# Optimization experiments

Measured on AMD Instinct MI355X. Metric: run time of the kernel, lower is better.

The kernel has to match this reference:

```python
import jax, jax.numpy as jnp
import numpy as np
from itertools import permutations

SIZES = (16, 32, 32, 32)  # token_sizes for layout dims (v, t, h, w)
N = SIZES[0] * SIZES[1] * SIZES[2] * SIZES[3]  # num_tokens = 524288
B = 32
EPS = 1e-3


def setup_inputs() -> dict:
    key = jax.random.key(0)
    ks = jax.random.split(key, 12)
    u = lambda k, shape: jax.random.uniform(k, shape, dtype=jnp.float32)
    alphas = [1.0, 2.0, 4.0]
    comps = np.array(
        [[alphas[v], alphas[t], alphas[hw], alphas[hw]]
         for v, t, hw in permutations(range(3), 3)], dtype=np.float32)  # [6, 4]
    return {
        "components": jnp.asarray(comps),
        "u_rate_src": u(ks[0], (1,)),
        "u_rate_tgt": u(ks[1], (1,)),
        "u0_src": u(ks[2], (B, N)),
        "u0_tgt": u(ks[3], (B, N)),
        "u_v_src": u(ks[4], (B, SIZES[0])),
        "u_t_src": u(ks[5], (B, SIZES[1])),
        "u_h_src": u(ks[6], (B, SIZES[2])),
        "u_w_src": u(ks[7], (B, SIZES[3])),
        "u_v_tgt": u(ks[8], (B, SIZES[0])),
        "u_t_tgt": u(ks[9], (B, SIZES[1])),
        "u_h_tgt": u(ks[10], (B, SIZES[2])),
        "u_w_tgt": u(ks[11], (B, SIZES[3])),
        "idx": 2,
    }


def _clamp(x):
    return jnp.clip(x, EPS, 1.0 - EPS)


def _binary_mask(u_rate, u0, u_dims, alphas):
    # event_prior: log-prob per token = log U0 + sum_dim log(U_dim)/alpha_dim (broadcast over pattern)
    P = jnp.log(_clamp(u0))  # [B, N]
    for i, ud in enumerate(u_dims):
        shape = [B, 1, 1, 1, 1]
        shape[1 + i] = SIZES[i]
        rep = jnp.broadcast_to(
            (jnp.log(_clamp(ud)) / alphas[i]).reshape(shape),
            (B,) + SIZES).reshape(B, N)
        P = P + rep
    # rate_prior: one shared uniform, K = floor(U * N), expanded over batch
    K = (_clamp(u_rate) * N).astype(jnp.int32)  # [1]
    K = jnp.broadcast_to(K, (B,))[:, None]  # [B, 1]
    # binary_topk_: rank via double argsort (0 = largest), mask = K > rank
    rank = jnp.argsort(jnp.argsort(-P, axis=-1), axis=-1)
    return K > rank


def reference(components, u_rate_src, u_rate_tgt, u0_src, u0_tgt,
              u_v_src, u_t_src, u_h_src, u_w_src,
              u_v_tgt, u_t_tgt, u_h_tgt, u_w_tgt, idx):
    alphas = components[idx]  # [4], one alpha per layout dim, shared by src/tgt
    src = _binary_mask(u_rate_src, u0_src,
                       (u_v_src, u_t_src, u_h_src, u_w_src), alphas)
    tgt = _binary_mask(u_rate_tgt, u0_tgt,
                       (u_v_tgt, u_t_tgt, u_h_tgt, u_w_tgt), alphas)
    return src, tgt
```

## Files before the change

kernel.cpp:

```cpp
#include <hip/hip_runtime.h>
#include <stdint.h>

#define NTOK 524288
#define ROWS 64
#define CHUNKS 64
#define NTHR 256
#define F4_PER_ROW (NTOK / 4)
#define F4_PER_CHUNK (F4_PER_ROW / CHUNKS)
#define F4_PER_THR (F4_PER_CHUNK / NTHR)
#define GCAP 8192
#define CB1CAP 131072
#define STAGECAP 2048
#define FB_CHUNKS 16

#define OFF_H1   0u
#define OFF_H2   (OFF_H1 + ROWS * 4096u * 4u)
#define OFF_B1   (OFF_H2 + ROWS * 4096u * 4u)
#define OFF_CG   (OFF_B1 + 256u)
#define OFF_B2   (OFF_CG + 256u)
#define OFF_REM  (OFF_B2 + 256u)
#define OFF_IT   (OFF_REM + 256u)
#define OFF_GCNT (OFF_IT + 256u)
#define OFF_BCNT (OFF_GCNT + 256u)
#define OFF_T    (OFF_BCNT + 256u)
#define OFF_ZERO_END (OFF_T + 512u)
#define OFF_TAB  OFF_ZERO_END
#define OFF_BK   (OFF_TAB + ROWS * 112u * 8u)
#define OFF_BI   (OFF_BK + (size_t)ROWS * CB1CAP * 8u)
#define OFF_GKEY (OFF_BI + (size_t)ROWS * CB1CAP * 4u)
#define OFF_GIDX (OFF_GKEY + (size_t)ROWS * GCAP * 8u)

__device__ __forceinline__ double clamp64(double x) {
  return fmin(fmax(x, 1.0e-3), 1.0 - 1.0e-3);
}

__device__ __forceinline__ unsigned compute_K(float ur) {
  float urf = fminf(fmaxf(ur, 1.0e-3f), 1.0f - 1.0e-3f);
  return (unsigned)(int)(urf * (float)NTOK);
}

__global__ void k_tables(const float* __restrict__ comps, const int* __restrict__ idxp,
                         const float* __restrict__ uvs, const float* __restrict__ uts,
                         const float* __restrict__ uhs, const float* __restrict__ uws,
                         const float* __restrict__ uvt, const float* __restrict__ utt,
                         const float* __restrict__ uht, const float* __restrict__ uwt,
                         double* __restrict__ tabs) {
  int idx = idxp[0];
  double alpha[4];
  for (int d = 0; d < 4; ++d) alpha[d] = (double)comps[idx * 4 + d];
  for (int i = threadIdx.x; i < ROWS * 112; i += blockDim.x) {
    int row = i / 112, j = i % 112;
    int m = row >> 5, b = row & 31;
    int d, jj, dsz;
    if (j < 16)      { d = 0; jj = j;      dsz = 16; }
    else if (j < 48) { d = 1; jj = j - 16; dsz = 32; }
    else if (j < 80) { d = 2; jj = j - 48; dsz = 32; }
    else             { d = 3; jj = j - 80; dsz = 32; }
    const float* u;
    if (m == 0) u = (d == 0) ? uvs : (d == 1) ? uts : (d == 2) ? uhs : uws;
    else        u = (d == 0) ? uvt : (d == 1) ? utt : (d == 2) ? uht : uwt;
    double x = clamp64((double)u[b * dsz + jj]);
    double a = alpha[d];
    double f;
    if (a == 1.0)      f = x;
    else if (a == 2.0) f = sqrt(x);
    else if (a == 4.0) f = sqrt(sqrt(x));
    else               f = pow(x, 1.0 / a);
    tabs[row * 112 + j] = f;
  }
}

__global__ void k_hist1(const float* __restrict__ u0s, const float* __restrict__ u0t,
                        const double* __restrict__ tabs, unsigned int* __restrict__ gh1) {
  __shared__ double tb[112];
  __shared__ unsigned int h[2 * 4100];
  int row = blockIdx.x / CHUNKS, chunk = blockIdx.x % CHUNKS;
  for (int i = threadIdx.x; i < 112; i += blockDim.x) tb[i] = tabs[row * 112 + i];
  for (int i = threadIdx.x; i < 2 * 4100; i += blockDim.x) h[i] = 0;
  __syncthreads();
  unsigned rep = (threadIdx.x & 1) * 4100u;
  int m = row >> 5, b = row & 31;
  const float4* u0 = reinterpret_cast<const float4*>((m ? u0t : u0s) + (size_t)b * NTOK);
  int base = chunk * F4_PER_CHUNK;
  for (int it = 0; it < F4_PER_THR; ++it) {
    int f4 = base + it * NTHR + threadIdx.x;
    float4 x = u0[f4];
    int n0 = f4 * 4;
    int w0 = n0 & 31, hh = (n0 >> 5) & 31, tt = (n0 >> 10) & 31, vv = n0 >> 15;
    double g = tb[vv] * tb[16 + tt] * tb[48 + hh];
    double k0 = clamp64((double)x.x) * (g * tb[80 + w0 + 0]);
    double k1 = clamp64((double)x.y) * (g * tb[80 + w0 + 1]);
    double k2 = clamp64((double)x.z) * (g * tb[80 + w0 + 2]);
    double k3 = clamp64((double)x.w) * (g * tb[80 + w0 + 3]);
    atomicAdd(&h[rep + ((unsigned)((unsigned long long)__double_as_longlong(k0) >> 51) & 0xFFFu)], 1u);
    atomicAdd(&h[rep + ((unsigned)((unsigned long long)__double_as_longlong(k1) >> 51) & 0xFFFu)], 1u);
    atomicAdd(&h[rep + ((unsigned)((unsigned long long)__double_as_longlong(k2) >> 51) & 0xFFFu)], 1u);
    atomicAdd(&h[rep + ((unsigned)((unsigned long long)__double_as_longlong(k3) >> 51) & 0xFFFu)], 1u);
  }
  __syncthreads();
  for (int i = threadIdx.x; i < 4096; i += blockDim.x) {
    unsigned c = h[i] + h[4100 + i];
    if (c) atomicAdd(&gh1[row * 4096 + i], c);
  }
}

__global__ __launch_bounds__(256) void k_scan1(const unsigned int* __restrict__ gh1,
                                               const float* __restrict__ urs,
                                               const float* __restrict__ urt,
                                               int* __restrict__ sB1, int* __restrict__ sCG) {
  __shared__ unsigned suf[256];
  __shared__ int best;
  int row = blockIdx.x;
  int t = threadIdx.x;
  const unsigned* h = gh1 + row * 4096;
  unsigned loc[16]; unsigned own = 0;
#pragma unroll
  for (int i = 0; i < 16; ++i) { loc[i] = h[t * 16 + i]; own += loc[i]; }
  suf[t] = own;
  if (t == 0) best = -1;
  __syncthreads();
  for (int off = 1; off < 256; off <<= 1) {
    unsigned add = (t + off < 256) ? suf[t + off] : 0u;
    __syncthreads();
    suf[t] += add;
    __syncthreads();
  }
  int m = row >> 5;
  unsigned K = compute_K(m ? urt[0] : urs[0]);
  unsigned above = suf[t] - own;
  int cand = -1;
  unsigned cum = above;
  for (int i = 15; i >= 0; --i) {
    if (cum + loc[i] >= K) { cand = t * 16 + i; break; }
    cum += loc[i];
  }
  if (cand >= 0) atomicMax(&best, cand);
  __syncthreads();
  int bb = best;
  if (bb >= 0 && (bb >> 4) == t) {
    unsigned cg = above;
    for (int i = 15; i > (bb & 15); --i) cg += loc[i];
    sB1[row] = bb;
    sCG[row] = (int)cg;
  }
}

__global__ void k_hist2g(const float* __restrict__ u0s, const float* __restrict__ u0t,
                         const double* __restrict__ tabs, const int* __restrict__ sB1,
                         unsigned int* __restrict__ gh2,
                         unsigned int* __restrict__ bcnt,
                         unsigned long long* __restrict__ bk, unsigned int* __restrict__ bi) {
  __shared__ double tb[112];
  __shared__ unsigned int h[4096];
  __shared__ unsigned long long sk[STAGECAP];
  __shared__ unsigned int si[STAGECAP];
  __shared__ unsigned int scnt;
  __shared__ unsigned int sbase;
  int row = blockIdx.x / CHUNKS, chunk = blockIdx.x % CHUNKS;
  for (int i = threadIdx.x; i < 112; i += blockDim.x) tb[i] = tabs[row * 112 + i];
  for (int i = threadIdx.x; i < 4096; i += blockDim.x) h[i] = 0;
  if (threadIdx.x == 0) scnt = 0;
  __syncthreads();
  unsigned b1 = (unsigned)sB1[row];
  int m = row >> 5, b = row & 31;
  const float4* u0 = reinterpret_cast<const float4*>((m ? u0t : u0s) + (size_t)b * NTOK);
  int base = chunk * F4_PER_CHUNK;
  for (int it = 0; it < F4_PER_THR; ++it) {
    int f4 = base + it * NTHR + threadIdx.x;
    float4 x = u0[f4];
    int n0 = f4 * 4;
    int w0 = n0 & 31, hh = (n0 >> 5) & 31, tt = (n0 >> 10) & 31, vv = n0 >> 15;
    double g = tb[vv] * tb[16 + tt] * tb[48 + hh];
    double ks[4];
    ks[0] = clamp64((double)x.x) * (g * tb[80 + w0 + 0]);
    ks[1] = clamp64((double)x.y) * (g * tb[80 + w0 + 1]);
    ks[2] = clamp64((double)x.z) * (g * tb[80 + w0 + 2]);
    ks[3] = clamp64((double)x.w) * (g * tb[80 + w0 + 3]);
#pragma unroll
    for (int c = 0; c < 4; ++c) {
      unsigned long long kb = (unsigned long long)__double_as_longlong(ks[c]);
      if (((unsigned)(kb >> 51) & 0xFFFu) == b1) {
        atomicAdd(&h[(unsigned)(kb >> 39) & 0xFFFu], 1u);
        unsigned p = atomicAdd(&scnt, 1u);
        if (p < STAGECAP) { sk[p] = kb; si[p] = (unsigned)(n0 + c); }
        else {
          unsigned gp = atomicAdd(&bcnt[row], 1u);
          if (gp < CB1CAP) {
            bk[(size_t)row * CB1CAP + gp] = kb;
            bi[(size_t)row * CB1CAP + gp] = (unsigned)(n0 + c);
          }
        }
      }
    }
  }
  __syncthreads();
  unsigned nst = scnt; if (nst > STAGECAP) nst = STAGECAP;
  if (threadIdx.x == 0) sbase = atomicAdd(&bcnt[row], nst);
  __syncthreads();
  unsigned bs = sbase;
  for (unsigned i = threadIdx.x; i < nst; i += blockDim.x) {
    unsigned gp = bs + i;
    if (gp < CB1CAP) {
      bk[(size_t)row * CB1CAP + gp] = sk[i];
      bi[(size_t)row * CB1CAP + gp] = si[i];
    }
  }
  for (int i = threadIdx.x; i < 4096; i += blockDim.x) {
    unsigned c = h[i];
    if (c) atomicAdd(&gh2[row * 4096 + i], c);
  }
}

__global__ __launch_bounds__(256) void k_scan2(const unsigned int* __restrict__ gh2,
                                               const float* __restrict__ urs,
                                               const float* __restrict__ urt,
                                               const int* __restrict__ sCG,
                                               int* __restrict__ sB2, int* __restrict__ sREM) {
  __shared__ unsigned suf[256];
  __shared__ int best;
  int row = blockIdx.x;
  int t = threadIdx.x;
  const unsigned* h = gh2 + row * 4096;
  unsigned loc[16]; unsigned own = 0;
#pragma unroll
  for (int i = 0; i < 16; ++i) { loc[i] = h[t * 16 + i]; own += loc[i]; }
  suf[t] = own;
  if (t == 0) best = -1;
  __syncthreads();
  for (int off = 1; off < 256; off <<= 1) {
    unsigned add = (t + off < 256) ? suf[t + off] : 0u;
    __syncthreads();
    suf[t] += add;
    __syncthreads();
  }
  int m = row >> 5;
  unsigned K = compute_K(m ? urt[0] : urs[0]);
  unsigned K2 = K - (unsigned)sCG[row];
  unsigned above = suf[t] - own;
  int cand = -1;
  unsigned cum = above;
  for (int i = 15; i >= 0; --i) {
    if (cum + loc[i] >= K2) { cand = t * 16 + i; break; }
    cum += loc[i];
  }
  if (cand >= 0) atomicMax(&best, cand);
  __syncthreads();
  int bb = best;
  if (bb >= 0 && (bb >> 4) == t) {
    unsigned a2 = above;
    for (int i = 15; i > (bb & 15); --i) a2 += loc[i];
    sB2[row] = bb;
    sREM[row] = (int)(K2 - a2);
  }
}

__global__ void k_gather_fb(const float* __restrict__ u0s, const float* __restrict__ u0t,
                            const double* __restrict__ tabs,
                            const int* __restrict__ sB1, const int* __restrict__ sB2,
                            const unsigned int* __restrict__ bcnt,
                            unsigned int* __restrict__ gcnt,
                            unsigned long long* __restrict__ gkey, unsigned int* __restrict__ gidx) {
  int row = blockIdx.x / FB_CHUNKS, chunk = blockIdx.x % FB_CHUNKS;
  if (bcnt[row] <= CB1CAP) return;
  __shared__ double tb[112];
  for (int i = threadIdx.x; i < 112; i += blockDim.x) tb[i] = tabs[row * 112 + i];
  __syncthreads();
  unsigned pref = ((unsigned)sB1[row] << 12) | (unsigned)sB2[row];
  int m = row >> 5, b = row & 31;
  const float4* u0 = reinterpret_cast<const float4*>((m ? u0t : u0s) + (size_t)b * NTOK);
  int base = chunk * (F4_PER_ROW / FB_CHUNKS);
  for (int it = 0; it < F4_PER_ROW / FB_CHUNKS / NTHR; ++it) {
    int f4 = base + it * NTHR + threadIdx.x;
    float4 x = u0[f4];
    int n0 = f4 * 4;
    int w0 = n0 & 31, hh = (n0 >> 5) & 31, tt = (n0 >> 10) & 31, vv = n0 >> 15;
    double g = tb[vv] * tb[16 + tt] * tb[48 + hh];
    double ks[4];
    ks[0] = clamp64((double)x.x) * (g * tb[80 + w0 + 0]);
    ks[1] = clamp64((double)x.y) * (g * tb[80 + w0 + 1]);
    ks[2] = clamp64((double)x.z) * (g * tb[80 + w0 + 2]);
    ks[3] = clamp64((double)x.w) * (g * tb[80 + w0 + 3]);
#pragma unroll
    for (int c = 0; c < 4; ++c) {
      unsigned long long kb = (unsigned long long)__double_as_longlong(ks[c]);
      if (((unsigned)(kb >> 39) & 0xFFFFFFu) == pref) {
        unsigned pos = atomicAdd(&gcnt[row], 1u);
        if (pos < GCAP) {
          gkey[(size_t)row * GCAP + pos] = kb;
          gidx[(size_t)row * GCAP + pos] = (unsigned)(n0 + c);
        }
      }
    }
  }
}

__global__ __launch_bounds__(1024) void k_select(const unsigned long long* __restrict__ bk,
                                                 const unsigned int* __restrict__ bi,
                                                 const unsigned int* __restrict__ bcnt,
                                                 const unsigned long long* __restrict__ gkey,
                                                 const unsigned int* __restrict__ gidx,
                                                 const unsigned int* __restrict__ gcnt,
                                                 const int* __restrict__ sB2,
                                                 const int* __restrict__ sREM,
                                                 unsigned long long* __restrict__ sT,
                                                 int* __restrict__ sIT) {
  __shared__ unsigned long long k[GCAP];
  __shared__ unsigned int ix[GCAP];
  __shared__ unsigned int lcnt;
  int row = blockIdx.x;
  if (threadIdx.x == 0) lcnt = 0;
  __syncthreads();
  unsigned cnt1 = bcnt[row];
  unsigned n_r;
  if (cnt1 <= CB1CAP) {
    unsigned b2 = (unsigned)sB2[row];
    for (unsigned i = threadIdx.x; i < cnt1; i += blockDim.x) {
      unsigned long long kb = bk[(size_t)row * CB1CAP + i];
      if (((unsigned)(kb >> 39) & 0xFFFu) == b2) {
        unsigned p = atomicAdd(&lcnt, 1u);
        if (p < GCAP) { k[p] = kb; ix[p] = bi[(size_t)row * CB1CAP + i]; }
      }
    }
    __syncthreads();
    n_r = lcnt; if (n_r > GCAP) n_r = GCAP;
  } else {
    n_r = gcnt[row];
    if (n_r > GCAP) n_r = GCAP;
    for (unsigned i = threadIdx.x; i < n_r; i += blockDim.x) {
      k[i] = gkey[(size_t)row * GCAP + i];
      ix[i] = gidx[(size_t)row * GCAP + i];
    }
    __syncthreads();
  }
  unsigned n2 = 2;
  while (n2 < n_r) n2 <<= 1;
  for (unsigned i = threadIdx.x; i < n2; i += blockDim.x) {
    if (i >= n_r) { k[i] = 0ULL; ix[i] = 0xFFFFFFFFu; }
  }
  __syncthreads();
  for (unsigned kk = 2; kk <= n2; kk <<= 1) {
    for (unsigned j = kk >> 1; j > 0; j >>= 1) {
      for (int i = threadIdx.x; i < (int)n2; i += blockDim.x) {
        int pj = i ^ (int)j;
        if (pj > i) {
          unsigned long long k1 = k[i], k2 = k[pj];
          unsigned i1 = ix[i], i2 = ix[pj];
          bool bef = (k1 > k2) || (k1 == k2 && i1 < i2);
          bool dirAsc = ((i & (int)kk) == 0);
          if (bef != dirAsc) { k[i] = k2; k[pj] = k1; ix[i] = i2; ix[pj] = i1; }
        }
      }
      __syncthreads();
    }
  }
  if (threadIdx.x == 0) {
    int rem = sREM[row];
    if (rem < 1) rem = 1;
    if ((unsigned)rem > n_r) rem = (int)n_r;
    sT[row] = k[rem - 1];
    sIT[row] = (int)ix[rem - 1];
  }
}

__global__ void k_final(const float* __restrict__ u0s, const float* __restrict__ u0t,
                        const double* __restrict__ tabs,
                        const unsigned long long* __restrict__ sT, const int* __restrict__ sIT,
                        int* __restrict__ out) {
  __shared__ double tb[112];
  int row = blockIdx.x / CHUNKS, chunk = blockIdx.x % CHUNKS;
  for (int i = threadIdx.x; i < 112; i += blockDim.x) tb[i] = tabs[row * 112 + i];
  __syncthreads();
  unsigned long long T = sT[row];
  int IT = sIT[row];
  int m = row >> 5, b = row & 31;
  const float4* u0 = reinterpret_cast<const float4*>((m ? u0t : u0s) + (size_t)b * NTOK);
  int4* o = reinterpret_cast<int4*>(out + (size_t)row * NTOK);
  int base = chunk * F4_PER_CHUNK;
  for (int it = 0; it < F4_PER_THR; ++it) {
    int f4 = base + it * NTHR + threadIdx.x;
    float4 x = u0[f4];
    int n0 = f4 * 4;
    int w0 = n0 & 31, hh = (n0 >> 5) & 31, tt = (n0 >> 10) & 31, vv = n0 >> 15;
    double g = tb[vv] * tb[16 + tt] * tb[48 + hh];
    unsigned long long kb0 = (unsigned long long)__double_as_longlong(clamp64((double)x.x) * (g * tb[80 + w0 + 0]));
    unsigned long long kb1 = (unsigned long long)__double_as_longlong(clamp64((double)x.y) * (g * tb[80 + w0 + 1]));
    unsigned long long kb2 = (unsigned long long)__double_as_longlong(clamp64((double)x.z) * (g * tb[80 + w0 + 2]));
    unsigned long long kb3 = (unsigned long long)__double_as_longlong(clamp64((double)x.w) * (g * tb[80 + w0 + 3]));
    int4 r;
    r.x = (kb0 > T || (kb0 == T && (n0 + 0) <= IT)) ? 1 : 0;
    r.y = (kb1 > T || (kb1 == T && (n0 + 1) <= IT)) ? 1 : 0;
    r.z = (kb2 > T || (kb2 == T && (n0 + 2) <= IT)) ? 1 : 0;
    r.w = (kb3 > T || (kb3 == T && (n0 + 3) <= IT)) ? 1 : 0;
    o[f4] = r;
  }
}

extern "C" void kernel_launch(void* const* d_in, const int* in_sizes, int n_in,
                              void* d_out, int out_size, void* d_ws, size_t ws_size,
                              hipStream_t stream) {
  const float* comps = (const float*)d_in[0];
  const float* urs   = (const float*)d_in[1];
  const float* urt   = (const float*)d_in[2];
  const float* u0s   = (const float*)d_in[3];
  const float* u0t   = (const float*)d_in[4];
  const float* uvs   = (const float*)d_in[5];
  const float* uts   = (const float*)d_in[6];
  const float* uhs   = (const float*)d_in[7];
  const float* uws   = (const float*)d_in[8];
  const float* uvt   = (const float*)d_in[9];
  const float* utt   = (const float*)d_in[10];
  const float* uht   = (const float*)d_in[11];
  const float* uwt   = (const float*)d_in[12];
  const int*   idxp  = (const int*)d_in[13];
  int* out = (int*)d_out;

  char* ws = (char*)d_ws;
  unsigned int*       gh1  = (unsigned int*)(ws + OFF_H1);
  unsigned int*       gh2  = (unsigned int*)(ws + OFF_H2);
  int*                sB1  = (int*)(ws + OFF_B1);
  int*                sCG  = (int*)(ws + OFF_CG);
  int*                sB2  = (int*)(ws + OFF_B2);
  int*                sREM = (int*)(ws + OFF_REM);
  int*                sIT  = (int*)(ws + OFF_IT);
  unsigned int*       gcnt = (unsigned int*)(ws + OFF_GCNT);
  unsigned int*       bcnt = (unsigned int*)(ws + OFF_BCNT);
  unsigned long long* sT   = (unsigned long long*)(ws + OFF_T);
  double*             tabs = (double*)(ws + OFF_TAB);
  unsigned long long* bk   = (unsigned long long*)(ws + OFF_BK);
  unsigned int*       bi   = (unsigned int*)(ws + OFF_BI);
  unsigned long long* gkey = (unsigned long long*)(ws + OFF_GKEY);
  unsigned int*       gidx = (unsigned int*)(ws + OFF_GIDX);

  hipMemsetAsync(d_ws, 0, OFF_ZERO_END, stream);

  k_tables<<<1, 256, 0, stream>>>(comps, idxp, uvs, uts, uhs, uws, uvt, utt, uht, uwt, tabs);
  k_hist1<<<ROWS * CHUNKS, NTHR, 0, stream>>>(u0s, u0t, tabs, gh1);
  k_scan1<<<ROWS, 256, 0, stream>>>(gh1, urs, urt, sB1, sCG);
  k_hist2g<<<ROWS * CHUNKS, NTHR, 0, stream>>>(u0s, u0t, tabs, sB1, gh2, bcnt, bk, bi);
  k_scan2<<<ROWS, 256, 0, stream>>>(gh2, urs, urt, sCG, sB2, sREM);
  k_gather_fb<<<ROWS * FB_CHUNKS, NTHR, 0, stream>>>(u0s, u0t, tabs, sB1, sB2, bcnt, gcnt, gkey, gidx);
  k_select<<<ROWS, 1024, 0, stream>>>(bk, bi, bcnt, gkey, gidx, gcnt, sB2, sREM, sT, sIT);
  k_final<<<ROWS * CHUNKS, NTHR, 0, stream>>>(u0s, u0t, tabs, sT, sIT, out);
}
```

Baseline: 401.4 us.

## Use finer offset 2048-bin first-pass radix histogram and direct candidate gather

The first radix pass now buckets keys by the top 17 bits of the double, offset and clamped into 2048 bins, instead of the top 12 bits. This makes the selected bucket much narrower, so fewer candidates are gathered and refined downstream, and the candidate buffer cap drops accordingly. The two-copy shared histogram is replaced by a single copy. The LDS staging of candidates is removed in favour of direct per-element global atomics and writes. These trade higher shared-atomic contention and per-candidate global atomics for a smaller candidate set. Clamping to edge bins could concentrate many keys into one bucket if the key range falls outside the assumed window.

```diff
diff --git a/kernel.cpp b/kernel.cpp
--- a/kernel.cpp
+++ b/kernel.cpp
@@ -8,26 +8,27 @@
 #define F4_PER_ROW (NTOK / 4)
 #define F4_PER_CHUNK (F4_PER_ROW / CHUNKS)
 #define F4_PER_THR (F4_PER_CHUNK / NTHR)
+#define NB1 2048
+#define B1BASE 30720
+#define BCAP 65536
 #define GCAP 8192
-#define CB1CAP 131072
-#define STAGECAP 2048
 #define FB_CHUNKS 16
 
-#define OFF_H1   0u
-#define OFF_H2   (OFF_H1 + ROWS * 4096u * 4u)
+#define OFF_H16  0u
+#define OFF_H2   (OFF_H16 + ROWS * NB1 * 4u)
 #define OFF_B1   (OFF_H2 + ROWS * 4096u * 4u)
 #define OFF_CG   (OFF_B1 + 256u)
 #define OFF_B2   (OFF_CG + 256u)
 #define OFF_REM  (OFF_B2 + 256u)
 #define OFF_IT   (OFF_REM + 256u)
-#define OFF_GCNT (OFF_IT + 256u)
-#define OFF_BCNT (OFF_GCNT + 256u)
-#define OFF_T    (OFF_BCNT + 256u)
+#define OFF_BCNT (OFF_IT + 256u)
+#define OFF_GCNT (OFF_BCNT + 256u)
+#define OFF_T    (OFF_GCNT + 256u)
 #define OFF_ZERO_END (OFF_T + 512u)
 #define OFF_TAB  OFF_ZERO_END
 #define OFF_BK   (OFF_TAB + ROWS * 112u * 8u)
-#define OFF_BI   (OFF_BK + (size_t)ROWS * CB1CAP * 8u)
-#define OFF_GKEY (OFF_BI + (size_t)ROWS * CB1CAP * 4u)
+#define OFF_BI   (OFF_BK + (size_t)ROWS * BCAP * 8u)
+#define OFF_GKEY (OFF_BI + (size_t)ROWS * BCAP * 4u)
 #define OFF_GIDX (OFF_GKEY + (size_t)ROWS * GCAP * 8u)
 
 __device__ __forceinline__ double clamp64(double x) {
@@ -37,6 +38,11 @@
 __device__ __forceinline__ unsigned compute_K(float ur) {
   float urf = fminf(fmaxf(ur, 1.0e-3f), 1.0f - 1.0e-3f);
   return (unsigned)(int)(urf * (float)NTOK);
+}
+
+__device__ __forceinline__ int bucket16(unsigned long long kb) {
+  int b = (int)(unsigned)(kb >> 47) - B1BASE;
+  return b < 0 ? 0 : (b > NB1 - 1 ? NB1 - 1 : b);
 }
 
 __global__ void k_tables(const float* __restrict__ comps, const int* __restrict__ idxp,
@@ -70,15 +76,14 @@
   }
 }
 
-__global__ void k_hist1(const float* __restrict__ u0s, const float* __restrict__ u0t,
-                        const double* __restrict__ tabs, unsigned int* __restrict__ gh1) {
+__global__ void k_hist16(const float* __restrict__ u0s, const float* __restrict__ u0t,
+                         const double* __restrict__ tabs, unsigned int* __restrict__ h16) {
   __shared__ double tb[112];
-  __shared__ unsigned int h[2 * 4100];
+  __shared__ unsigned int h[NB1];
   int row = blockIdx.x / CHUNKS, chunk = blockIdx.x % CHUNKS;
   for (int i = threadIdx.x; i < 112; i += blockDim.x) tb[i] = tabs[row * 112 + i];
-  for (int i = threadIdx.x; i < 2 * 4100; i += blockDim.x) h[i] = 0;
-  __syncthreads();
-  unsigned rep = (threadIdx.x & 1) * 4100u;
+  for (int i = threadIdx.x; i < NB1; i += blockDim.x) h[i] = 0;
+  __syncthreads();
   int m = row >> 5, b = row & 31;
   const float4* u0 = reinterpret_cast<const float4*>((m ? u0t : u0s) + (size_t)b * NTOK);
   int base = chunk * F4_PER_CHUNK;
@@ -92,30 +97,30 @@
     double k1 = clamp64((double)x.y) * (g * tb[80 + w0 + 1]);
     double k2 = clamp64((double)x.z) * (g * tb[80 + w0 + 2]);
     double k3 = clamp64((double)x.w) * (g * tb[80 + w0 + 3]);
-    atomicAdd(&h[rep + ((unsigned)((unsigned long long)__double_as_longlong(k0) >> 51) & 0xFFFu)], 1u);
-    atomicAdd(&h[rep + ((unsigned)((unsigned long long)__double_as_longlong(k1) >> 51) & 0xFFFu)], 1u);
-    atomicAdd(&h[rep + ((unsigned)((unsigned long long)__double_as_longlong(k2) >> 51) & 0xFFFu)], 1u);
-    atomicAdd(&h[rep + ((unsigned)((unsigned long long)__double_as_longlong(k3) >> 51) & 0xFFFu)], 1u);
-  }
-  __syncthreads();
-  for (int i = threadIdx.x; i < 4096; i += blockDim.x) {
-    unsigned c = h[i] + h[4100 + i];
-    if (c) atomicAdd(&gh1[row * 4096 + i], c);
-  }
-}
-
-__global__ __launch_bounds__(256) void k_scan1(const unsigned int* __restrict__ gh1,
-                                               const float* __restrict__ urs,
-                                               const float* __restrict__ urt,
-                                               int* __restrict__ sB1, int* __restrict__ sCG) {
+    atomicAdd(&h[bucket16((unsigned long long)__double_as_longlong(k0))], 1u);
+    atomicAdd(&h[bucket16((unsigned long long)__double_as_longlong(k1))], 1u);
+    atomicAdd(&h[bucket16((unsigned long long)__double_as_longlong(k2))], 1u);
+    atomicAdd(&h[bucket16((unsigned long long)__double_as_longlong(k3))], 1u);
+  }
+  __syncthreads();
+  for (int i = threadIdx.x; i < NB1; i += blockDim.x) {
+    unsigned c = h[i];
+    if (c) atomicAdd(&h16[row * NB1 + i], c);
+  }
+}
+
+__global__ __launch_bounds__(256) void k_scan16(const unsigned int* __restrict__ h16,
+                                                const float* __restrict__ urs,
+                                                const float* __restrict__ urt,
+                                                int* __restrict__ sB1, int* __restrict__ sCG) {
   __shared__ unsigned suf[256];
   __shared__ int best;
   int row = blockIdx.x;
   int t = threadIdx.x;
-  const unsigned* h = gh1 + row * 4096;
-  unsigned loc[16]; unsigned own = 0;
+  const unsigned* h = h16 + row * NB1;
+  unsigned loc[8]; unsigned own = 0;
 #pragma unroll
-  for (int i = 0; i < 16; ++i) { loc[i] = h[t * 16 + i]; own += loc[i]; }
+  for (int i = 0; i < 8; ++i) { loc[i] = h[t * 8 + i]; own += loc[i]; }
   suf[t] = own;
   if (t == 0) best = -1;
   __syncthreads();
@@ -130,38 +135,32 @@
   unsigned above = suf[t] - own;
   int cand = -1;
   unsigned cum = above;
-  for (int i = 15; i >= 0; --i) {
-    if (cum + loc[i] >= K) { cand = t * 16 + i; break; }
+  for (int i = 7; i >= 0; --i) {
+    if (cum + loc[i] >= K) { cand = t * 8 + i; break; }
     cum += loc[i];
   }
   if (cand >= 0) atomicMax(&best, cand);
   __syncthreads();
   int bb = best;
-  if (bb >= 0 && (bb >> 4) == t) {
+  if (bb >= 0 && (bb >> 3) == t) {
     unsigned cg = above;
-    for (int i = 15; i > (bb & 15); --i) cg += loc[i];
+    for (int i = 7; i > (bb & 7); --i) cg += loc[i];
     sB1[row] = bb;
     sCG[row] = (int)cg;
   }
 }
 
-__global__ void k_hist2g(const float* __restrict__ u0s, const float* __restrict__ u0t,
-                         const double* __restrict__ tabs, const int* __restrict__ sB1,
-                         unsigned int* __restrict__ gh2,
-                         unsigned int* __restrict__ bcnt,
-                         unsigned long long* __restrict__ bk, unsigned int* __restrict__ bi) {
+__global__ void k_gather2(const float* __restrict__ u0s, const float* __restrict__ u0t,
+                          const double* __restrict__ tabs, const int* __restrict__ sB1,
+                          unsigned int* __restrict__ gh2, unsigned int* __restrict__ bcnt,
+                          unsigned long long* __restrict__ bk, unsigned int* __restrict__ bi) {
   __shared__ double tb[112];
   __shared__ unsigned int h[4096];
-  __shared__ unsigned long long sk[STAGECAP];
-  __shared__ unsigned int si[STAGECAP];
-  __shared__ unsigned int scnt;
-  __shared__ unsigned int sbase;
   int row = blockIdx.x / CHUNKS, chunk = blockIdx.x % CHUNKS;
   for (int i = threadIdx.x; i < 112; i += blockDim.x) tb[i] = tabs[row * 112 + i];
   for (int i = threadIdx.x; i < 4096; i += blockDim.x) h[i] = 0;
-  if (threadIdx.x == 0) scnt = 0;
-  __syncthreads();
-  unsigned b1 = (unsigned)sB1[row];
+  __syncthreads();
+  int b1 = sB1[row];
   int m = row >> 5, b = row & 31;
   const float4* u0 = reinterpret_cast<const float4*>((m ? u0t : u0s) + (size_t)b * NTOK);
   int base = chunk * F4_PER_CHUNK;
@@ -179,32 +178,17 @@
 #pragma unroll
     for (int c = 0; c < 4; ++c) {
       unsigned long long kb = (unsigned long long)__double_as_longlong(ks[c]);
-      if (((unsigned)(kb >> 51) & 0xFFFu) == b1) {
+      if (bucket16(kb) == b1) {
         atomicAdd(&h[(unsigned)(kb >> 39) & 0xFFFu], 1u);
-        unsigned p = atomicAdd(&scnt, 1u);
-        if (p < STAGECAP) { sk[p] = kb; si[p] = (unsigned)(n0 + c); }
-        else {
-          unsigned gp = atomicAdd(&bcnt[row], 1u);
-          if (gp < CB1CAP) {
-            bk[(size_t)row * CB1CAP + gp] = kb;
-            bi[(size_t)row * CB1CAP + gp] = (unsigned)(n0 + c);
-          }
+        unsigned pos = atomicAdd(&bcnt[row], 1u);
+        if (pos < BCAP) {
+          bk[(size_t)row * BCAP + pos] = kb;
+          bi[(size_t)row * BCAP + pos] = (unsigned)(n0 + c);
         }
       }
     }
   }
   __syncthreads();
-  unsigned nst = scnt; if (nst > STAGECAP) nst = STAGECAP;
-  if (threadIdx.x == 0) sbase = atomicAdd(&bcnt[row], nst);
-  __syncthreads();
-  unsigned bs = sbase;
-  for (unsigned i = threadIdx.x; i < nst; i += blockDim.x) {
-    unsigned gp = bs + i;
-    if (gp < CB1CAP) {
-      bk[(size_t)row * CB1CAP + gp] = sk[i];
-      bi[(size_t)row * CB1CAP + gp] = si[i];
-    }
-  }
   for (int i = threadIdx.x; i < 4096; i += blockDim.x) {
     unsigned c = h[i];
     if (c) atomicAdd(&gh2[row * 4096 + i], c);
@@ -261,11 +245,12 @@
                             unsigned int* __restrict__ gcnt,
                             unsigned long long* __restrict__ gkey, unsigned int* __restrict__ gidx) {
   int row = blockIdx.x / FB_CHUNKS, chunk = blockIdx.x % FB_CHUNKS;
-  if (bcnt[row] <= CB1CAP) return;
+  if (bcnt[row] <= BCAP) return;
   __shared__ double tb[112];
   for (int i = threadIdx.x; i < 112; i += blockDim.x) tb[i] = tabs[row * 112 + i];
   __syncthreads();
-  unsigned pref = ((unsigned)sB1[row] << 12) | (unsigned)sB2[row];
+  int b1 = sB1[row];
+  unsigned b2 = (unsigned)sB2[row];
   int m = row >> 5, b = row & 31;
   const float4* u0 = reinterpret_cast<const float4*>((m ? u0t : u0s) + (size_t)b * NTOK);
   int base = chunk * (F4_PER_ROW / FB_CHUNKS);
@@ -283,7 +268,7 @@
 #pragma unroll
     for (int c = 0; c < 4; ++c) {
       unsigned long long kb = (unsigned long long)__double_as_longlong(ks[c]);
-      if (((unsigned)(kb >> 39) & 0xFFFFFFu) == pref) {
+      if (bucket16(kb) == b1 && (((unsigned)(kb >> 39)) & 0xFFFu) == b2) {
         unsigned pos = atomicAdd(&gcnt[row], 1u);
         if (pos < GCAP) {
           gkey[(size_t)row * GCAP + pos] = kb;
@@ -312,13 +297,13 @@
   __syncthreads();
   unsigned cnt1 = bcnt[row];
   unsigned n_r;
-  if (cnt1 <= CB1CAP) {
+  if (cnt1 <= BCAP) {
     unsigned b2 = (unsigned)sB2[row];
     for (unsigned i = threadIdx.x; i < cnt1; i += blockDim.x) {
-      unsigned long long kb = bk[(size_t)row * CB1CAP + i];
-      if (((unsigned)(kb >> 39) & 0xFFFu) == b2) {
+      unsigned long long kb = bk[(size_t)row * BCAP + i];
+      if ((((unsigned)(kb >> 39)) & 0xFFFu) == b2) {
         unsigned p = atomicAdd(&lcnt, 1u);
-        if (p < GCAP) { k[p] = kb; ix[p] = bi[(size_t)row * CB1CAP + i]; }
+        if (p < GCAP) { k[p] = kb; ix[p] = bi[(size_t)row * BCAP + i]; }
       }
     }
     __syncthreads();
@@ -415,15 +400,15 @@
   int* out = (int*)d_out;
 
   char* ws = (char*)d_ws;
-  unsigned int*       gh1  = (unsigned int*)(ws + OFF_H1);
+  unsigned int*       h16  = (unsigned int*)(ws + OFF_H16);
   unsigned int*       gh2  = (unsigned int*)(ws + OFF_H2);
   int*                sB1  = (int*)(ws + OFF_B1);
   int*                sCG  = (int*)(ws + OFF_CG);
   int*                sB2  = (int*)(ws + OFF_B2);
   int*                sREM = (int*)(ws + OFF_REM);
   int*                sIT  = (int*)(ws + OFF_IT);
+  unsigned int*       bcnt = (unsigned int*)(ws + OFF_BCNT);
   unsigned int*       gcnt = (unsigned int*)(ws + OFF_GCNT);
-  unsigned int*       bcnt = (unsigned int*)(ws + OFF_BCNT);
   unsigned long long* sT   = (unsigned long long*)(ws + OFF_T);
   double*             tabs = (double*)(ws + OFF_TAB);
   unsigned long long* bk   = (unsigned long long*)(ws + OFF_BK);
@@ -434,9 +419,9 @@
   hipMemsetAsync(d_ws, 0, OFF_ZERO_END, stream);
 
   k_tables<<<1, 256, 0, stream>>>(comps, idxp, uvs, uts, uhs, uws, uvt, utt, uht, uwt, tabs);
-  k_hist1<<<ROWS * CHUNKS, NTHR, 0, stream>>>(u0s, u0t, tabs, gh1);
-  k_scan1<<<ROWS, 256, 0, stream>>>(gh1, urs, urt, sB1, sCG);
-  k_hist2g<<<ROWS * CHUNKS, NTHR, 0, stream>>>(u0s, u0t, tabs, sB1, gh2, bcnt, bk, bi);
+  k_hist16<<<ROWS * CHUNKS, NTHR, 0, stream>>>(u0s, u0t, tabs, h16);
+  k_scan16<<<ROWS, 256, 0, stream>>>(h16, urs, urt, sB1, sCG);
+  k_gather2<<<ROWS * CHUNKS, NTHR, 0, stream>>>(u0s, u0t, tabs, sB1, gh2, bcnt, bk, bi);
   k_scan2<<<ROWS, 256, 0, stream>>>(gh2, urs, urt, sCG, sB2, sREM);
   k_gather_fb<<<ROWS * FB_CHUNKS, NTHR, 0, stream>>>(u0s, u0t, tabs, sB1, sB2, bcnt, gcnt, gkey, gidx);
   k_select<<<ROWS, 1024, 0, stream>>>(bk, bi, bcnt, gkey, gidx, gcnt, sB2, sREM, sT, sIT);
```

Result: slower. 657.1 us (+63.7%).
